# Kernel tuning notes

Measured on AMD Instinct MI355X. Metric: run time of the kernel, lower is better.

Reference implementation:

```python
import jax, jax.numpy as jnp
import numpy as np

N, E, G = 50000, 800000, 512
D_NODE, D_EDGE, D_HID, D_OUT = 64, 16, 64, 1


def _lin(key, din, dout, bias=True):
    k1, k2 = jax.random.split(key)
    w = jax.random.normal(k1, (din, dout), jnp.float32) / np.sqrt(din)
    if bias:
        b = jax.random.normal(k2, (dout,), jnp.float32) * 0.01
        return w, b
    return w


def setup_inputs() -> dict:
    key = jax.random.key(0)
    ks = jax.random.split(key, 24)
    x = jax.random.normal(ks[0], (N, D_NODE), jnp.float32)
    edge_index = jax.random.randint(ks[1], (2, E), 0, N, jnp.int64)
    edge_attr = jax.random.normal(ks[2], (E, D_EDGE), jnp.float32)
    batch = jnp.sort(jax.random.randint(ks[3], (N,), 0, G, jnp.int64))
    wq1, bq1 = _lin(ks[4], D_NODE, D_HID)
    wk1, bk1 = _lin(ks[5], D_NODE, D_HID)
    wv1, bv1 = _lin(ks[6], D_NODE, D_HID)
    we1 = _lin(ks[7], D_EDGE, D_HID, bias=False)
    ws1, bs1 = _lin(ks[8], D_NODE, D_HID)
    wq2, bq2 = _lin(ks[9], D_HID, D_HID)
    wk2, bk2 = _lin(ks[10], D_HID, D_HID)
    wv2, bv2 = _lin(ks[11], D_HID, D_HID)
    we2 = _lin(ks[12], D_EDGE, D_HID, bias=False)
    ws2, bs2 = _lin(ks[13], D_HID, D_HID)
    w_fc1, b_fc1 = _lin(ks[14], D_HID, D_HID)
    w_fc2, b_fc2 = _lin(ks[15], D_HID, D_OUT)
    return dict(x=x, edge_index=edge_index, edge_attr=edge_attr, batch=batch,
                wq1=wq1, bq1=bq1, wk1=wk1, bk1=bk1, wv1=wv1, bv1=bv1, we1=we1, ws1=ws1, bs1=bs1,
                wq2=wq2, bq2=bq2, wk2=wk2, bk2=bk2, wv2=wv2, bv2=bv2, we2=we2, ws2=ws2, bs2=bs2,
                w_fc1=w_fc1, b_fc1=b_fc1, w_fc2=w_fc2, b_fc2=b_fc2)


def _leaky(z):
    return jnp.where(z >= 0, z, 0.01 * z)


def _transformer_conv(x, src, dst, e, wq, bq, wk, bk, wv, bv, we, ws, bs):
    # PyG TransformerConv, heads=1, concat=True, root_weight=True
    C = wq.shape[1]
    q = x @ wq + bq                      # [N,C]
    k = x @ wk + bk                      # [N,C]
    v = x @ wv + bv                      # [N,C]
    ee = e @ we                          # [E,C] (lin_edge, bias=False)
    ke = k[src] + ee                     # per-edge key
    ve = v[src] + ee                     # per-edge value
    score = jnp.sum(q[dst] * ke, axis=-1) / jnp.sqrt(jnp.float32(C))  # [E]
    m = jax.ops.segment_max(score, dst, num_segments=N)
    a = jnp.exp(score - m[dst])
    den = jax.ops.segment_sum(a, dst, num_segments=N)
    den = jnp.where(den == 0, 1.0, den)
    alpha = a / den[dst]
    agg = jax.ops.segment_sum(alpha[:, None] * ve, dst, num_segments=N)
    return agg + x @ ws + bs             # skip connection


def reference(x, edge_index, edge_attr, batch,
              wq1, bq1, wk1, bk1, wv1, bv1, we1, ws1, bs1,
              wq2, bq2, wk2, bk2, wv2, bv2, we2, ws2, bs2,
              w_fc1, b_fc1, w_fc2, b_fc2):
    src, dst = edge_index[0], edge_index[1]
    h = _leaky(_transformer_conv(x, src, dst, edge_attr, wq1, bq1, wk1, bk1, wv1, bv1, we1, ws1, bs1))
    atom_embs = _leaky(_transformer_conv(h, src, dst, edge_attr, wq2, bq2, wk2, bk2, wv2, bv2, we2, ws2, bs2))
    pooled = jax.ops.segment_sum(atom_embs, batch, num_segments=G)    # [G,C]
    norm = jnp.linalg.norm(pooled, axis=1, keepdims=True)
    h = pooled / jnp.maximum(norm, 1e-12)                             # F.normalize p=2
    h = _leaky(h @ w_fc1 + b_fc1)
    out = h @ w_fc2 + b_fc2
    return (out, atom_embs)
```

## Files before the change

kernel.cpp:

```cpp
#include <hip/hip_runtime.h>
#include <hip/hip_bf16.h>
#include <math.h>


typedef unsigned int uint32;
typedef unsigned short u16;
typedef __attribute__((ext_vector_type(8))) short short8;
typedef __attribute__((ext_vector_type(4))) float f32x4;

__device__ __forceinline__ uint32 f2bf(float x) {
    uint32 u = __float_as_uint(x);
    u += 0x7fffu + ((u >> 16) & 1u);
    return u >> 16;
}
__device__ __forceinline__ float bf2f(u16 h) {
    return __uint_as_float(((uint32)h) << 16);
}


__global__ void hist_kernel(const int* __restrict__ dst, int* __restrict__ deg, int E) {
    int e = blockIdx.x * blockDim.x + threadIdx.x;
    if (e < E) atomicAdd(&deg[dst[e]], 1);
}

__global__ void scan1_kernel(const int* __restrict__ deg, int* __restrict__ row_ptr,
                             int* __restrict__ totals, int N) {
    __shared__ int sh[1024];
    int tid = threadIdx.x;
    int i = blockIdx.x * 1024 + tid;
    int d = (i < N) ? deg[i] : 0;
    int val = d;
    sh[tid] = val;
    __syncthreads();
    for (int off = 1; off < 1024; off <<= 1) {
        int add = (tid >= off) ? sh[tid - off] : 0;
        __syncthreads();
        val += add;
        sh[tid] = val;
        __syncthreads();
    }
    if (i < N) row_ptr[i] = val - d;
    if (tid == 1023) totals[blockIdx.x] = val;
}

__global__ void scan2_kernel(int* totals, int nb) {
    int lane = threadIdx.x;
    int v = (lane < nb) ? totals[lane] : 0;
    #pragma unroll
    for (int off = 1; off < 64; off <<= 1) {
        int t = __shfl_up(v, off);
        if (lane >= off) v += t;
    }
    int ex = __shfl_up(v, 1);
    if (lane == 0) ex = 0;
    if (lane < nb) totals[lane] = ex;
}

__global__ void scan3_kernel(int* __restrict__ row_ptr, const int* __restrict__ totals,
                             int N, int E) {
    int i = blockIdx.x * blockDim.x + threadIdx.x;
    if (i < N) row_ptr[i] += totals[i >> 10];
    if (i == 0) row_ptr[N] = E;
}

__global__ void scatter_kernel(const int* __restrict__ dst, const int* __restrict__ row_ptr,
                               int* __restrict__ fill, int* __restrict__ csr_eid, int E) {
    int e = blockIdx.x * blockDim.x + threadIdx.x;
    if (e < E) {
        int d = dst[e];
        int pos = row_ptr[d] + atomicAdd(&fill[d], 1);
        csr_eid[pos] = e;
    }
}

__global__ void convert_kernel(const int* __restrict__ csr_eid, const int* __restrict__ src,
                               const float* __restrict__ ea,
                               int* __restrict__ csr_src, u16* __restrict__ ea16, int E) {
    int p = blockIdx.x * blockDim.x + threadIdx.x;
    if (p >= E) return;
    int e = csr_eid[p];
    csr_src[p] = src[e];
    const float4* ev = (const float4*)(ea + (size_t)e * 16);
    float4 q0 = ev[0], q1 = ev[1], q2 = ev[2], q3 = ev[3];
    uint32* o = (uint32*)(ea16 + (size_t)p * 16);
    o[0] = f2bf(q0.x) | (f2bf(q0.y) << 16);
    o[1] = f2bf(q0.z) | (f2bf(q0.w) << 16);
    o[2] = f2bf(q1.x) | (f2bf(q1.y) << 16);
    o[3] = f2bf(q1.z) | (f2bf(q1.w) << 16);
    o[4] = f2bf(q2.x) | (f2bf(q2.y) << 16);
    o[5] = f2bf(q2.z) | (f2bf(q2.w) << 16);
    o[6] = f2bf(q3.x) | (f2bf(q3.y) << 16);
    o[7] = f2bf(q3.z) | (f2bf(q3.w) << 16);
}


__global__ void wprep_kernel(
    const float* __restrict__ wq1, const float* __restrict__ bq1,
    const float* __restrict__ wk1, const float* __restrict__ wv1,
    const float* __restrict__ ws1, const float* __restrict__ we1,
    const float* __restrict__ wq2, const float* __restrict__ bq2,
    const float* __restrict__ wk2, const float* __restrict__ wv2,
    const float* __restrict__ ws2, const float* __restrict__ we2,
    u16* __restrict__ wt1, float* __restrict__ be1,
    u16* __restrict__ wt2, float* __restrict__ be2)
{
    int L = blockIdx.x;
    const float* wq = L ? wq2 : wq1;
    const float* bq = L ? bq2 : bq1;
    const float* wk = L ? wk2 : wk1;
    const float* wv = L ? wv2 : wv1;
    const float* ws = L ? ws2 : ws1;
    const float* we = L ? we2 : we1;
    u16* wt = L ? wt2 : wt1;
    float* be = L ? be2 : be1;
    int t = threadIdx.x;
    for (int i = t; i < 4096; i += 256) {
        int k = i >> 6, n = i & 63;
        wt[0 * 4096 + n * 64 + k] = (u16)f2bf(wq[k * 64 + n]);
        wt[1 * 4096 + n * 64 + k] = (u16)f2bf(wk[k * 64 + n]);
        wt[2 * 4096 + n * 64 + k] = (u16)f2bf(wv[k * 64 + n]);
        wt[3 * 4096 + n * 64 + k] = (u16)f2bf(ws[k * 64 + n]);
    }
    for (int i = t; i < 1024; i += 256) {
        int j = i >> 6, k = i & 63;
        float acc = 0.f;
        for (int c = 0; c < 64; ++c) acc = fmaf(wq[k * 64 + c], we[j * 64 + c], acc);
        wt[4 * 4096 + j * 64 + k] = (u16)f2bf(acc * 0.125f);
    }
    if (t < 16) {
        float acc = 0.f;
        for (int c = 0; c < 64; ++c) acc = fmaf(bq[c], we[t * 64 + c], acc);
        be[t] = acc * 0.125f;
    }
}


__global__ __launch_bounds__(256) void qkvs_mfma(
    const float* __restrict__ xin, const u16* __restrict__ wt,
    const float* __restrict__ bq, const float* __restrict__ bk,
    const float* __restrict__ bv, const float* __restrict__ bs,
    const float* __restrict__ be,
    float* __restrict__ qo, uint32* __restrict__ kvo,
    float* __restrict__ so, float* __restrict__ qeo, int N)
{
    int wave = threadIdx.x >> 6;
    int lane = threadIdx.x & 63;
    int quad = lane >> 4;
    int l16 = lane & 15;
    int n0 = blockIdx.x * 64 + wave * 16;
    int row = n0 + l16;
    int rn = (row < N) ? row : (N - 1);

    const float4* xr = (const float4*)(xin + (size_t)rn * 64);
    float4 u0 = xr[quad * 2 + 0], u1 = xr[quad * 2 + 1];
    float4 u2 = xr[8 + quad * 2 + 0], u3 = xr[8 + quad * 2 + 1];
    short8 a0, a1;
    a0[0] = (short)f2bf(u0.x); a0[1] = (short)f2bf(u0.y);
    a0[2] = (short)f2bf(u0.z); a0[3] = (short)f2bf(u0.w);
    a0[4] = (short)f2bf(u1.x); a0[5] = (short)f2bf(u1.y);
    a0[6] = (short)f2bf(u1.z); a0[7] = (short)f2bf(u1.w);
    a1[0] = (short)f2bf(u2.x); a1[1] = (short)f2bf(u2.y);
    a1[2] = (short)f2bf(u2.z); a1[3] = (short)f2bf(u2.w);
    a1[4] = (short)f2bf(u3.x); a1[5] = (short)f2bf(u3.y);
    a1[6] = (short)f2bf(u3.z); a1[7] = (short)f2bf(u3.w);

    const short8* w8 = (const short8*)wt;

    f32x4 acc[4][4];
    #pragma unroll
    for (int m = 0; m < 4; ++m)
        #pragma unroll
        for (int c = 0; c < 4; ++c) acc[m][c] = (f32x4){0.f, 0.f, 0.f, 0.f};
    f32x4 aqe = (f32x4){0.f, 0.f, 0.f, 0.f};

    #pragma unroll
    for (int m = 0; m < 4; ++m) {
        #pragma unroll
        for (int c = 0; c < 4; ++c) {
            short8 b0 = w8[m * 512 + (c * 16 + l16) * 8 + quad];
            short8 b1 = w8[m * 512 + (c * 16 + l16) * 8 + 4 + quad];
            acc[m][c] = __builtin_amdgcn_mfma_f32_16x16x32_bf16(a0, b0, acc[m][c], 0, 0, 0);
            acc[m][c] = __builtin_amdgcn_mfma_f32_16x16x32_bf16(a1, b1, acc[m][c], 0, 0, 0);
        }
    }
    {
        short8 b0 = w8[4 * 512 + l16 * 8 + quad];
        short8 b1 = w8[4 * 512 + l16 * 8 + 4 + quad];
        aqe = __builtin_amdgcn_mfma_f32_16x16x32_bf16(a0, b0, aqe, 0, 0, 0);
        aqe = __builtin_amdgcn_mfma_f32_16x16x32_bf16(a1, b1, aqe, 0, 0, 0);
    }

    int node0 = n0 + quad * 4;
    #pragma unroll
    for (int c = 0; c < 4; ++c) {
        int col = c * 16 + l16;
        float bQ = bq[col], bK = bk[col], bV = bv[col], bS = bs[col];
        #pragma unroll
        for (int r = 0; r < 4; ++r) {
            int node = node0 + r;
            if (node < N) {
                size_t off = (size_t)node * 64 + col;
                qo[off] = (acc[0][c][r] + bQ) * 0.125f;
                kvo[off] = f2bf(acc[1][c][r] + bK) | (f2bf(acc[2][c][r] + bV) << 16);
                so[off] = acc[3][c][r] + bS;
            }
        }
    }
    float beL = be[l16];
    #pragma unroll
    for (int r = 0; r < 4; ++r) {
        int node = node0 + r;
        if (node < N) qeo[(size_t)node * 16 + l16] = aqe[r] + beL;
    }
}


__global__ __launch_bounds__(256) void agg_kernel(
    const float* __restrict__ q, const uint32* __restrict__ kv,
    const float* __restrict__ qe, const float* __restrict__ we,
    const u16* __restrict__ ea16,
    const int* __restrict__ row_ptr, const int* __restrict__ csr_src,
    const float* __restrict__ skip_in, float* __restrict__ hout,
    const int* __restrict__ batch, float* __restrict__ pooled, int N)
{
    int lane = threadIdx.x & 63;
    int wid = (blockIdx.x << 2) + (threadIdx.x >> 6);
    if (wid >= N) return;
    int i = __builtin_amdgcn_readfirstlane(wid);

    int grp = lane >> 4;
    int pos = lane & 15;

    float4 qv = ((const float4*)(q + (size_t)i * 64))[pos];
    float qel = qe[(size_t)i * 16 + pos];
    float wer[16];
    #pragma unroll
    for (int j = 0; j < 16; ++j) wer[j] = we[j * 64 + lane];

    float den = 0.f, aj = 0.f;
    float o4x = 0.f, o4y = 0.f, o4z = 0.f, o4w = 0.f;

    int beg = row_ptr[i], end = row_ptr[i + 1];
    int last = end - 1;
    for (int p = beg; p < end; p += 8) {
        int egA = p + grp, egB = p + 4 + grp;
        int siA = (egA < end) ? egA : last;
        int siB = (egB < end) ? egB : last;
        int sA = csr_src[siA], sB = csr_src[siB];
        uint4 kbA = ((const uint4*)(kv + (size_t)sA * 64))[pos];
        uint4 kbB = ((const uint4*)(kv + (size_t)sB * 64))[pos];
        float eaA = bf2f(ea16[(size_t)p * 16 + lane]);
        float eaB = bf2f(ea16[(size_t)(p + 4) * 16 + lane]);

        float pa = eaA * qel, pb = eaB * qel;
        pa = fmaf(qv.x, __uint_as_float(kbA.x << 16), pa);
        pb = fmaf(qv.x, __uint_as_float(kbB.x << 16), pb);
        pa = fmaf(qv.y, __uint_as_float(kbA.y << 16), pa);
        pb = fmaf(qv.y, __uint_as_float(kbB.y << 16), pb);
        pa = fmaf(qv.z, __uint_as_float(kbA.z << 16), pa);
        pb = fmaf(qv.z, __uint_as_float(kbB.z << 16), pb);
        pa = fmaf(qv.w, __uint_as_float(kbA.w << 16), pa);
        pb = fmaf(qv.w, __uint_as_float(kbB.w << 16), pb);
        pa += __shfl_xor(pa, 1);  pb += __shfl_xor(pb, 1);
        pa += __shfl_xor(pa, 2);  pb += __shfl_xor(pb, 2);
        pa += __shfl_xor(pa, 4);  pb += __shfl_xor(pb, 4);
        pa += __shfl_xor(pa, 8);  pb += __shfl_xor(pb, 8);
        float scA = (egA < end) ? pa : -1e30f;
        float scB = (egB < end) ? pb : -1e30f;
        float wA = __expf(scA), wB = __expf(scB);

        den += wA + wB;
        aj = fmaf(wA, eaA, aj);
        aj = fmaf(wB, eaB, aj);
        o4x = fmaf(wA, __uint_as_float(kbA.x & 0xffff0000u), o4x);
        o4y = fmaf(wA, __uint_as_float(kbA.y & 0xffff0000u), o4y);
        o4z = fmaf(wA, __uint_as_float(kbA.z & 0xffff0000u), o4z);
        o4w = fmaf(wA, __uint_as_float(kbA.w & 0xffff0000u), o4w);
        o4x = fmaf(wB, __uint_as_float(kbB.x & 0xffff0000u), o4x);
        o4y = fmaf(wB, __uint_as_float(kbB.y & 0xffff0000u), o4y);
        o4z = fmaf(wB, __uint_as_float(kbB.z & 0xffff0000u), o4z);
        o4w = fmaf(wB, __uint_as_float(kbB.w & 0xffff0000u), o4w);
    }

    o4x += __shfl_xor(o4x, 16); o4x += __shfl_xor(o4x, 32);
    o4y += __shfl_xor(o4y, 16); o4y += __shfl_xor(o4y, 32);
    o4z += __shfl_xor(o4z, 16); o4z += __shfl_xor(o4z, 32);
    o4w += __shfl_xor(o4w, 16); o4w += __shfl_xor(o4w, 32);
    aj  += __shfl_xor(aj, 16);  aj  += __shfl_xor(aj, 32);
    den += __shfl_xor(den, 16); den += __shfl_xor(den, 32);

    int srcl = lane >> 2;
    float t0 = __shfl(o4x, srcl), t1 = __shfl(o4y, srcl);
    float t2 = __shfl(o4z, srcl), t3 = __shfl(o4w, srcl);
    int r2 = lane & 3;
    float o = (r2 == 0) ? t0 : (r2 == 1) ? t1 : (r2 == 2) ? t2 : t3;

    #pragma unroll
    for (int j = 0; j < 16; ++j) o = fmaf(__shfl(aj, j), wer[j], o);

    float dinv = (den > 0.f) ? 1.f / den : 0.f;
    float r = fmaf(o, dinv, skip_in[(size_t)i * 64 + lane]);
    r = (r >= 0.f) ? r : 0.01f * r;
    hout[(size_t)i * 64 + lane] = r;
    if (pooled) atomicAdd(&pooled[(size_t)batch[i] * 64 + lane], r);
}


__global__ void head_kernel(const float* __restrict__ pooled,
                            const float* __restrict__ w1, const float* __restrict__ b1,
                            const float* __restrict__ w2, const float* __restrict__ b2,
                            float* __restrict__ out, int G) {
    int g = blockIdx.x;
    int lane = threadIdx.x;
    __shared__ float hl[64];
    float p = pooled[g * 64 + lane];
    float ss = p * p;
    #pragma unroll
    for (int off = 32; off; off >>= 1) ss += __shfl_xor(ss, off);
    float hn = p / fmaxf(sqrtf(ss), 1e-12f);
    hl[lane] = hn;
    __syncthreads();
    float acc = b1[lane];
    #pragma unroll
    for (int j = 0; j < 64; ++j) acc = fmaf(hl[j], w1[j * 64 + lane], acc);
    acc = (acc >= 0.f) ? acc : 0.01f * acc;
    float r = acc * w2[lane];
    #pragma unroll
    for (int off = 32; off; off >>= 1) r += __shfl_xor(r, off);
    if (lane == 0) out[g] = r + b2[0];
}


extern "C" void kernel_launch(void* const* d_in, const int* in_sizes, int n_in,
                              void* d_out, int out_size, void* d_ws, size_t ws_size,
                              hipStream_t stream) {
    const float* x     = (const float*)d_in[0];
    const int*   ei    = (const int*)  d_in[1];
    const float* ea    = (const float*)d_in[2];
    const int*   batch = (const int*)  d_in[3];
    const float *wq1=(const float*)d_in[4],  *bq1=(const float*)d_in[5];
    const float *wk1=(const float*)d_in[6],  *bk1=(const float*)d_in[7];
    const float *wv1=(const float*)d_in[8],  *bv1=(const float*)d_in[9];
    const float *we1=(const float*)d_in[10];
    const float *ws1=(const float*)d_in[11], *bs1=(const float*)d_in[12];
    const float *wq2=(const float*)d_in[13], *bq2=(const float*)d_in[14];
    const float *wk2=(const float*)d_in[15], *bk2=(const float*)d_in[16];
    const float *wv2=(const float*)d_in[17], *bv2=(const float*)d_in[18];
    const float *we2=(const float*)d_in[19];
    const float *ws2=(const float*)d_in[20], *bs2=(const float*)d_in[21];
    const float *wf1=(const float*)d_in[22], *bf1=(const float*)d_in[23];
    const float *wf2=(const float*)d_in[24], *bf2=(const float*)d_in[25];

    int N = in_sizes[0] / 64;
    int E = in_sizes[2] / 16;
    int G = out_size - N * 64;

    const int* srcA = ei;
    const int* dstA = ei + E;

    char* w = (char*)d_ws;
    float*  qb      = (float*)w;  w += (size_t)N * 64 * 4;
    uint32* kvb     = (uint32*)w; w += (size_t)N * 64 * 4;
    float*  hb      = (float*)w;  w += (size_t)N * 64 * 4;
    float*  qeb     = (float*)w;  w += (size_t)N * 16 * 4;
    float*  pooled  = (float*)w;  w += (size_t)G * 64 * 4;
    int* row_ptr    = (int*)w;    w += (size_t)(N + 1) * 4;
    int* totals     = (int*)w;    w += 256 * 4;
    u16* wt1        = (u16*)w;    w += (4 * 4096 + 1024) * 2;
    u16* wt2        = (u16*)w;    w += (4 * 4096 + 1024) * 2;
    float* be1      = (float*)w;  w += 16 * 4;
    float* be2      = (float*)w;  w += 16 * 4;
    int* csr_src    = (int*)w;    w += (size_t)E * 4;
    int* csr_eid    = (int*)w;    w += (size_t)E * 4;
    u16* ea16       = (u16*)w;    w += (size_t)(E * 16 + 128) * 2;
    int* deg  = (int*)qb;
    int* fill = (int*)qb + N;

    hipMemsetAsync(deg, 0, (size_t)2 * N * 4, stream);
    hipMemsetAsync(pooled, 0, (size_t)G * 64 * 4, stream);

    const int TB = 256;
    wprep_kernel<<<2, 256, 0, stream>>>(wq1, bq1, wk1, wv1, ws1, we1,
                                        wq2, bq2, wk2, wv2, ws2, we2,
                                        wt1, be1, wt2, be2);
    hist_kernel<<<(E + TB - 1) / TB, TB, 0, stream>>>(dstA, deg, E);
    int nb = (N + 1023) / 1024;
    scan1_kernel<<<nb, 1024, 0, stream>>>(deg, row_ptr, totals, N);
    scan2_kernel<<<1, 64, 0, stream>>>(totals, nb);
    scan3_kernel<<<(N + TB - 1) / TB, TB, 0, stream>>>(row_ptr, totals, N, E);
    scatter_kernel<<<(E + TB - 1) / TB, TB, 0, stream>>>(dstA, row_ptr, fill, csr_eid, E);
    convert_kernel<<<(E + TB - 1) / TB, TB, 0, stream>>>(csr_eid, srcA, ea,
                                                         csr_src, ea16, E);

    float* outp = (float*)d_out;
    float* atom = outp + G;

    int qBlocks = (N + 63) / 64;
    int aggBlocks = (N + 3) / 4;

    qkvs_mfma<<<qBlocks, 256, 0, stream>>>(x, wt1, bq1, bk1, bv1, bs1, be1,
                                           qb, kvb, hb, qeb, N);
    agg_kernel<<<aggBlocks, 256, 0, stream>>>(qb, kvb, qeb, we1, ea16, row_ptr, csr_src,
                                              hb, hb, nullptr, nullptr, N);

    qkvs_mfma<<<qBlocks, 256, 0, stream>>>(hb, wt2, bq2, bk2, bv2, bs2, be2,
                                           qb, kvb, atom, qeb, N);
    agg_kernel<<<aggBlocks, 256, 0, stream>>>(qb, kvb, qeb, we2, ea16, row_ptr, csr_src,
                                              atom, atom, batch, pooled, N);

    head_kernel<<<G, 64, 0, stream>>>(pooled, wf1, bf1, wf2, bf2, outp, G);
}
```

Baseline: 415.3 us.

## Build CSR via destination-bucketed two-pass sort and unroll aggregation by four

Replaces the histogram/three-kernel scan/global-atomic scatter/convert CSR construction with a bucketed approach: edges are appended into per-256-node buckets using shared-memory histograms, then each bucket is locally ranked to produce row_ptr and global positions, and a fill kernel writes csr_src and bf16 edge attributes. This cuts kernel launches and global atomic contention, and keeps the scatter writes local within a bucket. The aggregation loop now processes 16 edges per iteration in four groups instead of 8 in two, which raises memory-level parallelism. Risks: fixed bucket capacity CAP=5120 can overflow for skewed degree distributions, NB must be at most 256, and the edge index is packed into 20 bits, which limits E to about 1M; stable edge order is also lost.

```diff
diff --git a/kernel.cpp b/kernel.cpp
--- a/kernel.cpp
+++ b/kernel.cpp
@@ -8,6 +8,10 @@
 typedef __attribute__((ext_vector_type(8))) short short8;
 typedef __attribute__((ext_vector_type(4))) float f32x4;
 
+#define BW 256
+#define CAP 5120
+#define EPB 2048
+
 __device__ __forceinline__ uint32 f2bf(float x) {
     uint32 u = __float_as_uint(x);
     u += 0x7fffu + ((u >> 16) & 1u);
@@ -18,71 +22,99 @@
 }
 
 
-__global__ void hist_kernel(const int* __restrict__ dst, int* __restrict__ deg, int E) {
-    int e = blockIdx.x * blockDim.x + threadIdx.x;
-    if (e < E) atomicAdd(&deg[dst[e]], 1);
-}
-
-__global__ void scan1_kernel(const int* __restrict__ deg, int* __restrict__ row_ptr,
-                             int* __restrict__ totals, int N) {
-    __shared__ int sh[1024];
-    int tid = threadIdx.x;
-    int i = blockIdx.x * 1024 + tid;
-    int d = (i < N) ? deg[i] : 0;
-    int val = d;
-    sh[tid] = val;
-    __syncthreads();
-    for (int off = 1; off < 1024; off <<= 1) {
-        int add = (tid >= off) ? sh[tid - off] : 0;
+__global__ __launch_bounds__(256) void bucket_append(
+    const int* __restrict__ dst, const int* __restrict__ src,
+    int* __restrict__ bcount, uint2* __restrict__ buf, int E, int NB)
+{
+    __shared__ int hist[256], gbase[256], fill[256];
+    int t = threadIdx.x;
+    hist[t] = 0; fill[t] = 0;
+    __syncthreads();
+    int e0 = blockIdx.x * EPB;
+    int d[8], s[8];
+    #pragma unroll
+    for (int k = 0; k < 8; ++k) {
+        int e = e0 + k * 256 + t;
+        if (e < E) {
+            d[k] = dst[e]; s[k] = src[e];
+            atomicAdd(&hist[d[k] >> 8], 1);
+        } else d[k] = -1;
+    }
+    __syncthreads();
+    if (t < NB && hist[t] > 0) gbase[t] = atomicAdd(&bcount[t], hist[t]);
+    __syncthreads();
+    #pragma unroll
+    for (int k = 0; k < 8; ++k) {
+        if (d[k] >= 0) {
+            int e = e0 + k * 256 + t;
+            int b = d[k] >> 8;
+            int off = atomicAdd(&fill[b], 1);
+            buf[(size_t)b * CAP + gbase[b] + off] =
+                make_uint2(((uint32)(d[k] & 255) << 20) | (uint32)e, (uint32)s[k]);
+        }
+    }
+}
+
+__global__ __launch_bounds__(256) void csr_index(
+    const int* __restrict__ bcount, const uint2* __restrict__ buf,
+    int* __restrict__ row_ptr, int* __restrict__ gpos, int N, int E, int NB)
+{
+    __shared__ int sc[256], lh[256], lo[256], fill[256];
+    int t = threadIdx.x;
+    int b = blockIdx.x;
+    sc[t] = (t < NB) ? bcount[t] : 0;
+    lh[t] = 0; fill[t] = 0;
+    __syncthreads();
+    for (int off = 1; off < 256; off <<= 1) {
+        int add = (t >= off) ? sc[t - off] : 0;
         __syncthreads();
-        val += add;
-        sh[tid] = val;
+        sc[t] += add;
         __syncthreads();
     }
-    if (i < N) row_ptr[i] = val - d;
-    if (tid == 1023) totals[blockIdx.x] = val;
-}
-
-__global__ void scan2_kernel(int* totals, int nb) {
-    int lane = threadIdx.x;
-    int v = (lane < nb) ? totals[lane] : 0;
-    #pragma unroll
-    for (int off = 1; off < 64; off <<= 1) {
-        int t = __shfl_up(v, off);
-        if (lane >= off) v += t;
-    }
-    int ex = __shfl_up(v, 1);
-    if (lane == 0) ex = 0;
-    if (lane < nb) totals[lane] = ex;
-}
-
-__global__ void scan3_kernel(int* __restrict__ row_ptr, const int* __restrict__ totals,
-                             int N, int E) {
-    int i = blockIdx.x * blockDim.x + threadIdx.x;
-    if (i < N) row_ptr[i] += totals[i >> 10];
-    if (i == 0) row_ptr[N] = E;
-}
-
-__global__ void scatter_kernel(const int* __restrict__ dst, const int* __restrict__ row_ptr,
-                               int* __restrict__ fill, int* __restrict__ csr_eid, int E) {
-    int e = blockIdx.x * blockDim.x + threadIdx.x;
-    if (e < E) {
-        int d = dst[e];
-        int pos = row_ptr[d] + atomicAdd(&fill[d], 1);
-        csr_eid[pos] = e;
-    }
-}
-
-__global__ void convert_kernel(const int* __restrict__ csr_eid, const int* __restrict__ src,
-                               const float* __restrict__ ea,
-                               int* __restrict__ csr_src, u16* __restrict__ ea16, int E) {
-    int p = blockIdx.x * blockDim.x + threadIdx.x;
-    if (p >= E) return;
-    int e = csr_eid[p];
-    csr_src[p] = src[e];
+    int cnt = bcount[b];
+    int base = sc[b] - cnt;
+
+    const uint2* bb = buf + (size_t)b * CAP;
+    for (int i = t; i < cnt; i += 256) atomicAdd(&lh[(int)(bb[i].x >> 20)], 1);
+    __syncthreads();
+    int v = lh[t];
+    lo[t] = v;
+    __syncthreads();
+    for (int off = 1; off < 256; off <<= 1) {
+        int add = (t >= off) ? lo[t - off] : 0;
+        __syncthreads();
+        lo[t] += add;
+        __syncthreads();
+    }
+    int ex = lo[t] - v;
+    int d = b * BW + t;
+    if (d < N) row_ptr[d] = base + ex;
+    if (b == 0 && t == 0) row_ptr[N] = E;
+    lo[t] = ex;
+    __syncthreads();
+    for (int i = t; i < cnt; i += 256) {
+        int dl = (int)(bb[i].x >> 20);
+        int off = atomicAdd(&fill[dl], 1);
+        gpos[(size_t)b * CAP + i] = base + lo[dl] + off;
+    }
+}
+
+__global__ __launch_bounds__(256) void csr_fill(
+    const int* __restrict__ bcount, const uint2* __restrict__ buf,
+    const int* __restrict__ gpos, const float* __restrict__ ea,
+    int* __restrict__ csr_src, u16* __restrict__ ea16)
+{
+    int b = blockIdx.y;
+    int slot = blockIdx.x * 256 + threadIdx.x;
+    if (slot >= bcount[b]) return;
+    size_t idx = (size_t)b * CAP + slot;
+    uint2 ent = buf[idx];
+    int gp = gpos[idx];
+    csr_src[gp] = (int)ent.y;
+    int e = (int)(ent.x & 0xFFFFFu);
     const float4* ev = (const float4*)(ea + (size_t)e * 16);
     float4 q0 = ev[0], q1 = ev[1], q2 = ev[2], q3 = ev[3];
-    uint32* o = (uint32*)(ea16 + (size_t)p * 16);
+    uint32* o = (uint32*)(ea16 + (size_t)gp * 16);
     o[0] = f2bf(q0.x) | (f2bf(q0.y) << 16);
     o[1] = f2bf(q0.z) | (f2bf(q0.w) << 16);
     o[2] = f2bf(q1.x) | (f2bf(q1.y) << 16);
@@ -242,44 +274,32 @@
 
     int beg = row_ptr[i], end = row_ptr[i + 1];
     int last = end - 1;
-    for (int p = beg; p < end; p += 8) {
-        int egA = p + grp, egB = p + 4 + grp;
-        int siA = (egA < end) ? egA : last;
-        int siB = (egB < end) ? egB : last;
-        int sA = csr_src[siA], sB = csr_src[siB];
-        uint4 kbA = ((const uint4*)(kv + (size_t)sA * 64))[pos];
-        uint4 kbB = ((const uint4*)(kv + (size_t)sB * 64))[pos];
-        float eaA = bf2f(ea16[(size_t)p * 16 + lane]);
-        float eaB = bf2f(ea16[(size_t)(p + 4) * 16 + lane]);
-
-        float pa = eaA * qel, pb = eaB * qel;
-        pa = fmaf(qv.x, __uint_as_float(kbA.x << 16), pa);
-        pb = fmaf(qv.x, __uint_as_float(kbB.x << 16), pb);
-        pa = fmaf(qv.y, __uint_as_float(kbA.y << 16), pa);
-        pb = fmaf(qv.y, __uint_as_float(kbB.y << 16), pb);
-        pa = fmaf(qv.z, __uint_as_float(kbA.z << 16), pa);
-        pb = fmaf(qv.z, __uint_as_float(kbB.z << 16), pb);
-        pa = fmaf(qv.w, __uint_as_float(kbA.w << 16), pa);
-        pb = fmaf(qv.w, __uint_as_float(kbB.w << 16), pb);
-        pa += __shfl_xor(pa, 1);  pb += __shfl_xor(pb, 1);
-        pa += __shfl_xor(pa, 2);  pb += __shfl_xor(pb, 2);
-        pa += __shfl_xor(pa, 4);  pb += __shfl_xor(pb, 4);
-        pa += __shfl_xor(pa, 8);  pb += __shfl_xor(pb, 8);
-        float scA = (egA < end) ? pa : -1e30f;
-        float scB = (egB < end) ? pb : -1e30f;
-        float wA = __expf(scA), wB = __expf(scB);
-
-        den += wA + wB;
-        aj = fmaf(wA, eaA, aj);
-        aj = fmaf(wB, eaB, aj);
-        o4x = fmaf(wA, __uint_as_float(kbA.x & 0xffff0000u), o4x);
-        o4y = fmaf(wA, __uint_as_float(kbA.y & 0xffff0000u), o4y);
-        o4z = fmaf(wA, __uint_as_float(kbA.z & 0xffff0000u), o4z);
-        o4w = fmaf(wA, __uint_as_float(kbA.w & 0xffff0000u), o4w);
-        o4x = fmaf(wB, __uint_as_float(kbB.x & 0xffff0000u), o4x);
-        o4y = fmaf(wB, __uint_as_float(kbB.y & 0xffff0000u), o4y);
-        o4z = fmaf(wB, __uint_as_float(kbB.z & 0xffff0000u), o4z);
-        o4w = fmaf(wB, __uint_as_float(kbB.w & 0xffff0000u), o4w);
+    for (int p = beg; p < end; p += 16) {
+        #pragma unroll
+        for (int c = 0; c < 4; ++c) {
+            int eg = p + 4 * c + grp;
+            int si = (eg < end) ? eg : last;
+            int s = csr_src[si];
+            uint4 kb = ((const uint4*)(kv + (size_t)s * 64))[pos];
+            float eav = bf2f(ea16[(size_t)(p + 4 * c) * 16 + lane]);
+            float pa = eav * qel;
+            pa = fmaf(qv.x, __uint_as_float(kb.x << 16), pa);
+            pa = fmaf(qv.y, __uint_as_float(kb.y << 16), pa);
+            pa = fmaf(qv.z, __uint_as_float(kb.z << 16), pa);
+            pa = fmaf(qv.w, __uint_as_float(kb.w << 16), pa);
+            pa += __shfl_xor(pa, 1);
+            pa += __shfl_xor(pa, 2);
+            pa += __shfl_xor(pa, 4);
+            pa += __shfl_xor(pa, 8);
+            float sc = (eg < end) ? pa : -1e30f;
+            float w = __expf(sc);
+            den += w;
+            aj = fmaf(w, eav, aj);
+            o4x = fmaf(w, __uint_as_float(kb.x & 0xffff0000u), o4x);
+            o4y = fmaf(w, __uint_as_float(kb.y & 0xffff0000u), o4y);
+            o4z = fmaf(w, __uint_as_float(kb.z & 0xffff0000u), o4z);
+            o4w = fmaf(w, __uint_as_float(kb.w & 0xffff0000u), o4w);
+        }
     }
 
     o4x += __shfl_xor(o4x, 16); o4x += __shfl_xor(o4x, 32);
@@ -354,6 +374,7 @@
     int N = in_sizes[0] / 64;
     int E = in_sizes[2] / 16;
     int G = out_size - N * 64;
+    int NB = (N + BW - 1) / BW;
 
     const int* srcA = ei;
     const int* dstA = ei + E;
@@ -364,33 +385,26 @@
     float*  hb      = (float*)w;  w += (size_t)N * 64 * 4;
     float*  qeb     = (float*)w;  w += (size_t)N * 16 * 4;
     float*  pooled  = (float*)w;  w += (size_t)G * 64 * 4;
+    int* bcount     = (int*)w;    w += 256 * 4;
     int* row_ptr    = (int*)w;    w += (size_t)(N + 1) * 4;
-    int* totals     = (int*)w;    w += 256 * 4;
     u16* wt1        = (u16*)w;    w += (4 * 4096 + 1024) * 2;
     u16* wt2        = (u16*)w;    w += (4 * 4096 + 1024) * 2;
     float* be1      = (float*)w;  w += 16 * 4;
     float* be2      = (float*)w;  w += 16 * 4;
     int* csr_src    = (int*)w;    w += (size_t)E * 4;
-    int* csr_eid    = (int*)w;    w += (size_t)E * 4;
-    u16* ea16       = (u16*)w;    w += (size_t)(E * 16 + 128) * 2;
-    int* deg  = (int*)qb;
-    int* fill = (int*)qb + N;
-
-    hipMemsetAsync(deg, 0, (size_t)2 * N * 4, stream);
-    hipMemsetAsync(pooled, 0, (size_t)G * 64 * 4, stream);
-
-    const int TB = 256;
+    u16* ea16       = (u16*)w;    w += ((size_t)E * 16 + 1024) * 2;
+    uint2* bbuf     = (uint2*)w;  w += (size_t)NB * CAP * 8;
+    int* gpos       = (int*)w;    w += (size_t)NB * CAP * 4;
+
+    hipMemsetAsync(pooled, 0, (size_t)G * 64 * 4 + 256 * 4, stream);
+
     wprep_kernel<<<2, 256, 0, stream>>>(wq1, bq1, wk1, wv1, ws1, we1,
                                         wq2, bq2, wk2, wv2, ws2, we2,
                                         wt1, be1, wt2, be2);
-    hist_kernel<<<(E + TB - 1) / TB, TB, 0, stream>>>(dstA, deg, E);
-    int nb = (N + 1023) / 1024;
-    scan1_kernel<<<nb, 1024, 0, stream>>>(deg, row_ptr, totals, N);
-    scan2_kernel<<<1, 64, 0, stream>>>(totals, nb);
-    scan3_kernel<<<(N + TB - 1) / TB, TB, 0, stream>>>(row_ptr, totals, N, E);
-    scatter_kernel<<<(E + TB - 1) / TB, TB, 0, stream>>>(dstA, row_ptr, fill, csr_eid, E);
-    convert_kernel<<<(E + TB - 1) / TB, TB, 0, stream>>>(csr_eid, srcA, ea,
-                                                         csr_src, ea16, E);
+    bucket_append<<<(E + EPB - 1) / EPB, 256, 0, stream>>>(dstA, srcA, bcount, bbuf, E, NB);
+    csr_index<<<NB, 256, 0, stream>>>(bcount, bbuf, row_ptr, gpos, N, E, NB);
+    csr_fill<<<dim3(CAP / 256, NB), 256, 0, stream>>>(bcount, bbuf, gpos, ea,
+                                                      csr_src, ea16);
 
     float* outp = (float*)d_out;
     float* atom = outp + G;
```

Result: faster. 381.0 us (-8.3%).
